# Optimization experiments

Hardware: AMD Instinct MI355X
Metric: run time of the kernel (lower is better)

Reference implementation:

```python
import jax, jax.numpy as jnp
import numpy as np

ALPHA = 0.9

def setup_inputs() -> dict:
    key = jax.random.key(0)
    k1, k2 = jax.random.split(key)
    x = jax.random.normal(k1, (1024, 32, 1024), dtype=jnp.float32)
    state = jax.random.normal(k2, (32, 1024), dtype=jnp.float32)
    return {"x": x, "state": state}

def reference(x, state):
    # EMA recurrence: s_t = alpha * s_{t-1} + (1 - alpha) * x_t
    def step(s, xt):
        s = xt * (1.0 - ALPHA) + s * ALPHA
        return s, s
    final_state, out = jax.lax.scan(step, state, x)
    return out, final_state
```

## Files before the change

kernel.cpp:

```cpp
#include <hip/hip_runtime.h>


typedef float f32x4 __attribute__((ext_vector_type(4)));

constexpr int T = 1024;
constexpr int C = 32 * 1024;
constexpr int CV = C / 4;
constexpr int CHUNK = 64;
constexpr int NCHUNK = T / CHUNK;
constexpr int WARM = 64;
constexpr int G = 8;

__global__ __launch_bounds__(256)
void ExponentialDecay_23708219474744_kernel(const f32x4* __restrict__ x4,
                                            const f32x4* __restrict__ state4,
                                            f32x4* __restrict__ out4) {
    const int cv = blockIdx.x * blockDim.x + threadIdx.x;
    const int chunk = blockIdx.y;
    const int t0 = chunk * CHUNK;
    const float a = 0.9f;
    const float oma = 0.1f;

    f32x4 s = {};
    int tb;
    if (chunk == 0) {
        s = state4[cv];
        tb = 0;
    } else {
        tb = t0 - WARM;
    }

    const int nit = (chunk == 0) ? CHUNK : (CHUNK + WARM);
    const int ng = nit / G;
    const int gstore = (t0 - tb) / G;

    const f32x4* __restrict__ xp = x4 + (size_t)tb * CV + cv;
    f32x4* __restrict__ op = out4 + (size_t)t0 * CV + cv;

    f32x4 cur[G], nxt[G];
    #pragma unroll
    for (int i = 0; i < G; ++i) cur[i] = xp[(size_t)i * CV];

    for (int g = 0; g < ng; ++g) {
        if (g + 1 < ng) {
            const f32x4* __restrict__ xn = xp + (size_t)(g + 1) * G * CV;
            #pragma unroll
            for (int i = 0; i < G; ++i) nxt[i] = xn[(size_t)i * CV];
        }

        if (g >= gstore) {
            f32x4* o = op + (size_t)(g - gstore) * G * CV;
            #pragma unroll
            for (int i = 0; i < G; ++i) {
                f32x4 v = cur[i];
                s.x = fmaf(s.x, a, v.x * oma);
                s.y = fmaf(s.y, a, v.y * oma);
                s.z = fmaf(s.z, a, v.z * oma);
                s.w = fmaf(s.w, a, v.w * oma);
                __builtin_nontemporal_store(s, o + (size_t)i * CV);
            }
        } else {
            #pragma unroll
            for (int i = 0; i < G; ++i) {
                f32x4 v = cur[i];
                s.x = fmaf(s.x, a, v.x * oma);
                s.y = fmaf(s.y, a, v.y * oma);
                s.z = fmaf(s.z, a, v.z * oma);
                s.w = fmaf(s.w, a, v.w * oma);
            }
        }

        if (g + 1 < ng) {
            #pragma unroll
            for (int i = 0; i < G; ++i) cur[i] = nxt[i];
        }
    }

    if (chunk == NCHUNK - 1) {
        out4[(size_t)T * CV + cv] = s;
    }
}

extern "C" void kernel_launch(void* const* d_in, const int* in_sizes, int n_in,
                              void* d_out, int out_size, void* d_ws, size_t ws_size,
                              hipStream_t stream) {
    const f32x4* x = (const f32x4*)d_in[0];
    const f32x4* state = (const f32x4*)d_in[1];
    f32x4* out = (f32x4*)d_out;

    dim3 block(256);
    dim3 grid(CV / 256, NCHUNK);
    ExponentialDecay_23708219474744_kernel<<<grid, block, 0, stream>>>(x, state, out);
}
```

Measured before the change: 254.9 us.

## Replace warmup-overlap chunking with exact two-pass chunked scan

Splits the recurrence into a first kernel that computes each chunk's local end state from zero and a second kernel that combines the previous chunks' local states using alpha^64 to get an exact starting state, then rescans its chunk and writes outputs. This removes the redundant 64-step warmup reads per chunk and the approximation they imply. It adds a second kernel launch, a workspace round trip, and a serial prefix loop over earlier chunks, and it replaces the nontemporal stores with regular stores.

Result: no change. 255.8 us (+0.4%).

```diff
diff --git a/kernel.cpp b/kernel.cpp
--- a/kernel.cpp
+++ b/kernel.cpp
@@ -8,75 +8,60 @@
 constexpr int CV = C / 4;
 constexpr int CHUNK = 64;
 constexpr int NCHUNK = T / CHUNK;
-constexpr int WARM = 64;
-constexpr int G = 8;
+constexpr float A64 = 1.1790184577738602e-3f;
+
+__global__ __launch_bounds__(256)
+void ExponentialDecay_23708219474744_locals(const f32x4* __restrict__ x4,
+                                            f32x4* __restrict__ L) {
+    const int cv = blockIdx.x * blockDim.x + threadIdx.x;
+    const int c = blockIdx.y;
+    const f32x4* __restrict__ xp = x4 + (size_t)c * CHUNK * CV + cv;
+
+    const float a = 0.9f, oma = 0.1f;
+    f32x4 s = {0.0f, 0.0f, 0.0f, 0.0f};
+    #pragma unroll 8
+    for (int t = 0; t < CHUNK; ++t) {
+        f32x4 v = xp[(size_t)t * CV];
+        s.x = fmaf(s.x, a, v.x * oma);
+        s.y = fmaf(s.y, a, v.y * oma);
+        s.z = fmaf(s.z, a, v.z * oma);
+        s.w = fmaf(s.w, a, v.w * oma);
+    }
+    L[(size_t)c * CV + cv] = s;
+}
 
 __global__ __launch_bounds__(256)
 void ExponentialDecay_23708219474744_kernel(const f32x4* __restrict__ x4,
                                             const f32x4* __restrict__ state4,
+                                            const f32x4* __restrict__ L,
                                             f32x4* __restrict__ out4) {
     const int cv = blockIdx.x * blockDim.x + threadIdx.x;
-    const int chunk = blockIdx.y;
-    const int t0 = chunk * CHUNK;
-    const float a = 0.9f;
-    const float oma = 0.1f;
+    const int c = blockIdx.y;
+    const float a = 0.9f, oma = 0.1f;
 
-    f32x4 s = {};
-    int tb;
-    if (chunk == 0) {
-        s = state4[cv];
-        tb = 0;
-    } else {
-        tb = t0 - WARM;
+    f32x4 s = state4[cv];
+    for (int j = 0; j < c; ++j) {
+        f32x4 l = L[(size_t)j * CV + cv];
+        s.x = fmaf(s.x, A64, l.x);
+        s.y = fmaf(s.y, A64, l.y);
+        s.z = fmaf(s.z, A64, l.z);
+        s.w = fmaf(s.w, A64, l.w);
     }
 
-    const int nit = (chunk == 0) ? CHUNK : (CHUNK + WARM);
-    const int ng = nit / G;
-    const int gstore = (t0 - tb) / G;
+    const f32x4* __restrict__ xp = x4 + (size_t)c * CHUNK * CV + cv;
+    f32x4* __restrict__ op = out4 + (size_t)c * CHUNK * CV + cv;
 
-    const f32x4* __restrict__ xp = x4 + (size_t)tb * CV + cv;
-    f32x4* __restrict__ op = out4 + (size_t)t0 * CV + cv;
-
-    f32x4 cur[G], nxt[G];
-    #pragma unroll
-    for (int i = 0; i < G; ++i) cur[i] = xp[(size_t)i * CV];
-
-    for (int g = 0; g < ng; ++g) {
-        if (g + 1 < ng) {
-            const f32x4* __restrict__ xn = xp + (size_t)(g + 1) * G * CV;
-            #pragma unroll
-            for (int i = 0; i < G; ++i) nxt[i] = xn[(size_t)i * CV];
-        }
-
-        if (g >= gstore) {
-            f32x4* o = op + (size_t)(g - gstore) * G * CV;
-            #pragma unroll
-            for (int i = 0; i < G; ++i) {
-                f32x4 v = cur[i];
-                s.x = fmaf(s.x, a, v.x * oma);
-                s.y = fmaf(s.y, a, v.y * oma);
-                s.z = fmaf(s.z, a, v.z * oma);
-                s.w = fmaf(s.w, a, v.w * oma);
-                __builtin_nontemporal_store(s, o + (size_t)i * CV);
-            }
-        } else {
-            #pragma unroll
-            for (int i = 0; i < G; ++i) {
-                f32x4 v = cur[i];
-                s.x = fmaf(s.x, a, v.x * oma);
-                s.y = fmaf(s.y, a, v.y * oma);
-                s.z = fmaf(s.z, a, v.z * oma);
-                s.w = fmaf(s.w, a, v.w * oma);
-            }
-        }
-
-        if (g + 1 < ng) {
-            #pragma unroll
-            for (int i = 0; i < G; ++i) cur[i] = nxt[i];
-        }
+    #pragma unroll 8
+    for (int t = 0; t < CHUNK; ++t) {
+        f32x4 v = xp[(size_t)t * CV];
+        s.x = fmaf(s.x, a, v.x * oma);
+        s.y = fmaf(s.y, a, v.y * oma);
+        s.z = fmaf(s.z, a, v.z * oma);
+        s.w = fmaf(s.w, a, v.w * oma);
+        op[(size_t)t * CV] = s;
     }
 
-    if (chunk == NCHUNK - 1) {
+    if (c == NCHUNK - 1) {
         out4[(size_t)T * CV + cv] = s;
     }
 }
@@ -87,8 +72,12 @@
     const f32x4* x = (const f32x4*)d_in[0];
     const f32x4* state = (const f32x4*)d_in[1];
     f32x4* out = (f32x4*)d_out;
+    f32x4* L = (f32x4*)d_ws;
 
     dim3 block(256);
-    dim3 grid(CV / 256, NCHUNK);
-    ExponentialDecay_23708219474744_kernel<<<grid, block, 0, stream>>>(x, state, out);
+    dim3 grid1(CV / 256, NCHUNK - 1);
+    ExponentialDecay_23708219474744_locals<<<grid1, block, 0, stream>>>(x, L);
+
+    dim3 grid2(CV / 256, NCHUNK);
+    ExponentialDecay_23708219474744_kernel<<<grid2, block, 0, stream>>>(x, state, L, out);
 }
```
